# Kernel tuning notes

Measured on AMD Instinct MI355X. Metric: run time of the kernel, lower is better.

## Reference

```python
import jax, jax.numpy as jnp
import numpy as np

EPS = 1e-5
D_STATE = 16
D_INNER = 2
D_CONV = 4


def batchnorm(x, g, b):
    # BatchNorm1d in training mode: biased batch statistics over the batch dim
    m = x.mean(axis=0)
    v = x.var(axis=0)
    return g * (x - m) * jax.lax.rsqrt(v + EPS) + b


def mamba(u, W_in, conv_w, conv_b, W_xproj, W_dt, b_dt, A_log, D, W_out):
    # u: [B, L, 1] (d_model=1, d_inner=2, d_state=16, dt_rank=1)
    Bsz, L, _ = u.shape
    xz = jnp.einsum('bld,ed->ble', u, W_in)            # [B,L,4]
    x, z = jnp.split(xz, 2, axis=-1)                    # [B,L,2] each
    # causal depthwise conv along L
    xc = jnp.transpose(x, (0, 2, 1))                    # [B,C,L]
    xc = jax.lax.conv_general_dilated(
        xc, conv_w, (1,), [(D_CONV - 1, 0)],
        dimension_numbers=('NCH', 'OIH', 'NCH'),
        feature_group_count=D_INNER)
    x = jax.nn.silu(jnp.transpose(xc, (0, 2, 1)) + conv_b)  # [B,L,2]
    x_dbl = jnp.einsum('ble,fe->blf', x, W_xproj)       # [B,L,1+2*16]
    dt = jax.nn.softplus(jnp.einsum('blr,er->ble', x_dbl[..., :1], W_dt) + b_dt)  # [B,L,2]
    Bm = x_dbl[..., 1:1 + D_STATE]                      # [B,L,16]
    Cm = x_dbl[..., 1 + D_STATE:1 + 2 * D_STATE]        # [B,L,16]
    A = -jnp.exp(A_log)                                 # [2,16]

    def step(h, inp):
        dt_t, B_t, C_t, x_t = inp                       # [B,2],[B,16],[B,16],[B,2]
        dA = jnp.exp(dt_t[:, :, None] * A)              # [B,2,16]
        h = h * dA + dt_t[:, :, None] * B_t[:, None, :] * x_t[:, :, None]
        y = jnp.einsum('ben,bn->be', h, C_t) + D * x_t
        return h, y

    h0 = jnp.zeros((Bsz, D_INNER, D_STATE), u.dtype)
    xs = (dt.transpose(1, 0, 2), Bm.transpose(1, 0, 2),
          Cm.transpose(1, 0, 2), x.transpose(1, 0, 2))
    _, ys = jax.lax.scan(step, h0, xs)                  # [L,B,2]
    y = ys.transpose(1, 0, 2) * jax.nn.silu(z)          # [B,L,2]
    return jnp.einsum('ble,de->bld', y, W_out)          # [B,L,1]


def setup_inputs() -> dict:
    key = jax.random.key(0)
    ks = jax.random.split(key, 16)
    B = 1024
    s = 0.02
    inp = {
        'x': jax.random.normal(ks[0], (B, 1775), jnp.float32),
        'W1': jax.random.normal(ks[1], (2048, 1775), jnp.float32) * s,
        'g1': jnp.ones((2048,), jnp.float32),
        'b1': jnp.zeros((2048,), jnp.float32),
        'W_in': jax.random.normal(ks[2], (2 * D_INNER, 1), jnp.float32) * s,
        'conv_w': jax.random.normal(ks[3], (D_INNER, 1, D_CONV), jnp.float32) * 0.2,
        'conv_b': jnp.zeros((D_INNER,), jnp.float32),
        'W_xproj': jax.random.normal(ks[4], (1 + 2 * D_STATE, D_INNER), jnp.float32) * 0.2,
        'W_dt': jax.random.normal(ks[5], (D_INNER, 1), jnp.float32) * 0.2,
        'b_dt': jax.random.normal(ks[6], (D_INNER,), jnp.float32) * 0.2,
        'A_log': jnp.tile(jnp.log(jnp.arange(1, D_STATE + 1, dtype=jnp.float32)), (D_INNER, 1)),
        'D': jnp.ones((D_INNER,), jnp.float32),
        'W_out': jax.random.normal(ks[7], (1, D_INNER), jnp.float32) * 0.2,
        'W2': jax.random.normal(ks[8], (512, 2048), jnp.float32) * s,
        'g2': jnp.ones((512,), jnp.float32),
        'b2': jnp.zeros((512,), jnp.float32),
        'W3': jax.random.normal(ks[9], (256, 512), jnp.float32) * s,
    }
    return inp


def reference(x, W1, g1, b1, W_in, conv_w, conv_b, W_xproj, W_dt, b_dt,
              A_log, D, W_out, W2, g2, b2, W3):
    h = batchnorm(x @ W1.T, g1, b1)                     # [B,2048]
    h = mamba(h[:, :, None], W_in, conv_w, conv_b, W_xproj, W_dt, b_dt,
              A_log, D, W_out)[:, :, 0]                 # [B,2048]
    h = jax.nn.relu(batchnorm(h @ W2.T, g2, b2))        # [B,512]
    return h @ W3.T                                     # [B,256]
```

## Files before the change

kernel.cpp:

```cpp
#include <hip/hip_runtime.h>
#include <math.h>

#define SEQL 2048
#define BATCH 1024
#define CHUNK 64
#define NCH 32

typedef _Float16 f16x8 __attribute__((ext_vector_type(8)));
typedef _Float16 f16x4 __attribute__((ext_vector_type(4)));
typedef _Float16 h2 __attribute__((ext_vector_type(2)));
typedef float f32x4 __attribute__((ext_vector_type(4)));

__device__ inline unsigned short f2h(float f) {
    _Float16 h = (_Float16)f;
    return *reinterpret_cast<unsigned short*>(&h);
}
__device__ inline float packh2(float a, float b) {
    return __uint_as_float((unsigned)f2h(a) | ((unsigned)f2h(b) << 16));
}
__device__ inline float hext(float packed, int sh) {
    const unsigned short s = (unsigned short)(__float_as_uint(packed) >> sh);
    _Float16 h = *reinterpret_cast<const _Float16*>(&s);
    return (float)h;
}

__device__ inline void gl2lds16(const void* g, void* l) {
    __builtin_amdgcn_global_load_lds(
        (const __attribute__((address_space(1))) unsigned int*)g,
        (__attribute__((address_space(3))) unsigned int*)l, 16, 0, 0);
}

template<int CTRL>
__device__ inline float dppadd(float v) {
    const int p = __builtin_amdgcn_update_dpp(0, __float_as_int(v), CTRL, 0xF, 0xF, true);
    return v + __int_as_float(p);
}

__global__ __launch_bounds__(256) void cvt_all(
    const float* __restrict__ x, const float* __restrict__ W1,
    const float* __restrict__ W2, const float* __restrict__ W3,
    _Float16* __restrict__ xh, _Float16* __restrict__ w1h,
    _Float16* __restrict__ w2h, _Float16* __restrict__ w3h)
{
    const int bid = blockIdx.x;
    if (bid < 3072) {
        const float* src; _Float16* dst;
        if (bid < 1024) { src = x + (size_t)bid * 1775;           dst = xh  + (size_t)bid * 1792; }
        else            { src = W1 + (size_t)(bid - 1024) * 1775; dst = w1h + (size_t)(bid - 1024) * 1792; }
        f16x4* dst4 = reinterpret_cast<f16x4*>(dst);
        for (int i = threadIdx.x; i < 448; i += 256) {
            const int k = i * 4;
            float4 v = {0.f, 0.f, 0.f, 0.f};
            if (k + 3 < 1775) v = *reinterpret_cast<const float4*>(&src[k]);
            else {
                if (k     < 1775) v.x = src[k];
                if (k + 1 < 1775) v.y = src[k + 1];
                if (k + 2 < 1775) v.z = src[k + 2];
            }
            f16x4 o; o[0] = (_Float16)v.x; o[1] = (_Float16)v.y; o[2] = (_Float16)v.z; o[3] = (_Float16)v.w;
            dst4[i] = o;
        }
    } else {
        const float* src; _Float16* dst; int nvec;
        if (bid < 3584) { const int r = bid - 3072; src = W2 + (size_t)r * 2048; dst = w2h + (size_t)r * 2048; nvec = 512; }
        else            { const int r = bid - 3584; src = W3 + (size_t)r * 512;  dst = w3h + (size_t)r * 512;  nvec = 128; }
        f16x4* dst4 = reinterpret_cast<f16x4*>(dst);
        for (int i = threadIdx.x; i < nvec; i += 256) {
            const float4 v = reinterpret_cast<const float4*>(src)[i];
            f16x4 o; o[0] = (_Float16)v.x; o[1] = (_Float16)v.y; o[2] = (_Float16)v.z; o[3] = (_Float16)v.w;
            dst4[i] = o;
        }
    }
}

__global__ __launch_bounds__(256) void cvt_bnrelu(
    const float* __restrict__ P0, const float* __restrict__ P1,
    const float* __restrict__ sc, const float* __restrict__ tc,
    _Float16* __restrict__ h3)
{
    const int row = blockIdx.x * 2 + (threadIdx.x >> 7);
    const int i = threadIdx.x & 127;
    const float4 p0 = reinterpret_cast<const float4*>(P0 + (size_t)row * 512)[i];
    const float4 p1 = reinterpret_cast<const float4*>(P1 + (size_t)row * 512)[i];
    const float4 sv = reinterpret_cast<const float4*>(sc)[i];
    const float4 tv = reinterpret_cast<const float4*>(tc)[i];
    f16x4 o;
    o[0] = (_Float16)fmaxf(fmaf(sv.x, p0.x + p1.x, tv.x), 0.f);
    o[1] = (_Float16)fmaxf(fmaf(sv.y, p0.y + p1.y, tv.y), 0.f);
    o[2] = (_Float16)fmaxf(fmaf(sv.z, p0.z + p1.z, tv.z), 0.f);
    o[3] = (_Float16)fmaxf(fmaf(sv.w, p0.w + p1.w, tv.w), 0.f);
    reinterpret_cast<f16x4*>(h3 + (size_t)row * 512)[i] = o;
}

__global__ __launch_bounds__(256) void gemm_f16(
    const _Float16* __restrict__ A, const _Float16* __restrict__ B,
    float* __restrict__ C, int ldc, int Kp, int ksteps, size_t coff,
    float* __restrict__ bnp, int bn_ld)
{
    __shared__ __attribute__((aligned(16))) _Float16 sA[2][64 * 64];
    __shared__ __attribute__((aligned(16))) _Float16 sB[2][64 * 64];

    const int tid = threadIdx.x;
    const int wave = tid >> 6;
    const int lane = tid & 63;
    const int m0 = blockIdx.y * 64;
    const int n0 = blockIdx.x * 64;
    C += (size_t)blockIdx.z * coff;

    const int srow = tid >> 3;
    const int pslot = tid & 7;
    const int gslot = pslot ^ (srow & 7);
    const size_t gk0 = (size_t)blockIdx.z * ksteps * 64 + (size_t)gslot * 8;
    const _Float16* gA0 = A + (size_t)(m0 + srow) * Kp + gk0;
    const _Float16* gA1 = A + (size_t)(m0 + 32 + srow) * Kp + gk0;
    const _Float16* gB0 = B + (size_t)(n0 + srow) * Kp + gk0;
    const _Float16* gB1 = B + (size_t)(n0 + 32 + srow) * Kp + gk0;
    const int wdst = wave * 512;

    const int wr = wave >> 1, wc = wave & 1;
    const int li = lane & 15, gq = lane >> 4;
    const int p0s = (gq    ) ^ (li & 7);
    const int p1s = (gq + 4) ^ (li & 7);

    f32x4 acc[2][2];
    #pragma unroll
    for (int i = 0; i < 2; ++i)
        #pragma unroll
        for (int j = 0; j < 2; ++j)
            #pragma unroll
            for (int v = 0; v < 4; ++v) acc[i][j][v] = 0.f;

    gl2lds16(gA0, &sA[0][wdst]);
    gl2lds16(gA1, &sA[0][2048 + wdst]);
    gl2lds16(gB0, &sB[0][wdst]);
    gl2lds16(gB1, &sB[0][2048 + wdst]);
    __syncthreads();

    int cur = 0;
    for (int kt = 0; kt < ksteps; ++kt) {
        if (kt + 1 < ksteps) {
            const size_t go = (size_t)(kt + 1) * 64;
            const int nb = cur ^ 1;
            gl2lds16(gA0 + go, &sA[nb][wdst]);
            gl2lds16(gA1 + go, &sA[nb][2048 + wdst]);
            gl2lds16(gB0 + go, &sB[nb][wdst]);
            gl2lds16(gB1 + go, &sB[nb][2048 + wdst]);
        }

        f16x8 af[2][2], bg[2][2];
        #pragma unroll
        for (int mi = 0; mi < 2; ++mi) {
            const int rb = (wr * 32 + mi * 16 + li) * 64;
            af[mi][0] = *(const f16x8*)&sA[cur][rb + p0s * 8];
            af[mi][1] = *(const f16x8*)&sA[cur][rb + p1s * 8];
        }
        #pragma unroll
        for (int ni = 0; ni < 2; ++ni) {
            const int rb = (wc * 32 + ni * 16 + li) * 64;
            bg[ni][0] = *(const f16x8*)&sB[cur][rb + p0s * 8];
            bg[ni][1] = *(const f16x8*)&sB[cur][rb + p1s * 8];
        }
        #pragma unroll
        for (int mi = 0; mi < 2; ++mi)
            #pragma unroll
            for (int ni = 0; ni < 2; ++ni) {
                acc[mi][ni] = __builtin_amdgcn_mfma_f32_16x16x32_f16(af[mi][0], bg[ni][0], acc[mi][ni], 0, 0, 0);
                acc[mi][ni] = __builtin_amdgcn_mfma_f32_16x16x32_f16(af[mi][1], bg[ni][1], acc[mi][ni], 0, 0, 0);
            }
        __syncthreads();
        cur ^= 1;
    }

    #pragma unroll
    for (int mi = 0; mi < 2; ++mi)
        #pragma unroll
        for (int ni = 0; ni < 2; ++ni) {
            const int col = n0 + wc * 32 + ni * 16 + li;
            #pragma unroll
            for (int i = 0; i < 4; ++i) {
                const int row = m0 + wr * 32 + mi * 16 + gq * 4 + i;
                C[(size_t)row * ldc + col] = acc[mi][ni][i];
            }
        }

    if (bnp) {
        #pragma unroll
        for (int ni = 0; ni < 2; ++ni) {
            float ps = 0.f, pq = 0.f;
            #pragma unroll
            for (int mi = 0; mi < 2; ++mi)
                #pragma unroll
                for (int i = 0; i < 4; ++i) {
                    const float v = acc[mi][ni][i];
                    ps += v; pq += v * v;
                }
            ps += __shfl_xor(ps, 16); ps += __shfl_xor(ps, 32);
            pq += __shfl_xor(pq, 16); pq += __shfl_xor(pq, 32);
            if (gq == 0) {
                const int col = n0 + wc * 32 + ni * 16 + li;
                const int grp = blockIdx.y * 2 + wr;
                bnp[(size_t)(grp * 2    ) * bn_ld + col] = ps;
                bnp[(size_t)(grp * 2 + 1) * bn_ld + col] = pq;
            }
        }
    }
}

__global__ __launch_bounds__(256) void bn_part(
    const float* __restrict__ X, const float* __restrict__ X2,
    int rows_per, int ld, float* __restrict__ part)
{
    __shared__ float rs[4][64], rq[4][64];
    const int tid = threadIdx.x;
    const int c = tid & 63, rg4 = tid >> 6;
    const int col = blockIdx.x * 64 + c;
    const int r0 = blockIdx.y * rows_per;
    float sum = 0.f, sq = 0.f;
    for (int r = rg4; r < rows_per; r += 4) {
        const size_t idx = (size_t)(r0 + r) * ld + col;
        float v = X[idx];
        if (X2) v += X2[idx];
        sum += v; sq += v * v;
    }
    rs[rg4][c] = sum; rq[rg4][c] = sq;
    __syncthreads();
    if (rg4 == 0) {
        sum = rs[0][c] + rs[1][c] + rs[2][c] + rs[3][c];
        sq  = rq[0][c] + rq[1][c] + rq[2][c] + rq[3][c];
        part[((size_t)blockIdx.y * 2    ) * ld + col] = sum;
        part[((size_t)blockIdx.y * 2 + 1) * ld + col] = sq;
    }
}

__global__ __launch_bounds__(256) void bn_fin(
    const float* __restrict__ part, int RG, int ld, float inv_rows,
    const float* __restrict__ g, const float* __restrict__ b,
    float* __restrict__ s, float* __restrict__ t)
{
    const int col = blockIdx.x * 256 + threadIdx.x;
    if (col >= ld) return;
    float sum = 0.f, sq = 0.f;
    for (int z = 0; z < RG; ++z) {
        sum += part[((size_t)z * 2    ) * ld + col];
        sq  += part[((size_t)z * 2 + 1) * ld + col];
    }
    const float mean = sum * inv_rows;
    const float var = fmaxf(sq * inv_rows - mean * mean, 0.f);
    const float rstd = 1.0f / sqrtf(var + 1e-5f);
    const float sv = g[col] * rstd;
    s[col] = sv;
    t[col] = b[col] - mean * sv;
}

__global__ __launch_bounds__(512, 8) void mamba_scan9(
    const float* __restrict__ Y, _Float16* __restrict__ a2,
    const float* __restrict__ s1, const float* __restrict__ t1,
    const float* __restrict__ Win, const float* __restrict__ convw,
    const float* __restrict__ convb, const float* __restrict__ Wx,
    const float* __restrict__ Wdt, const float* __restrict__ bdt,
    const float* __restrict__ Alog, const float* __restrict__ Dp,
    const float* __restrict__ Wout)
{
    __shared__ __align__(16) float4 pk[SEQL];
    __shared__ float Pa[2][NCH][16];
    __shared__ float Sa[2][NCH][16];

    const int tid = threadIdx.x;
    const int row = blockIdx.x;
    const float* yrow = Y + (size_t)row * SEQL;
    _Float16* a2row = a2 + (size_t)row * SEQL;

    {
        const int l0 = tid * 4;
        float4 ym = {0.f,0.f,0.f,0.f}, sm = {0.f,0.f,0.f,0.f}, tm = {0.f,0.f,0.f,0.f};
        if (tid > 0) {
            ym = *reinterpret_cast<const float4*>(&yrow[l0 - 4]);
            sm = *reinterpret_cast<const float4*>(&s1[l0 - 4]);
            tm = *reinterpret_cast<const float4*>(&t1[l0 - 4]);
        }
        const float4 y0 = *reinterpret_cast<const float4*>(&yrow[l0]);
        const float4 s0 = *reinterpret_cast<const float4*>(&s1[l0]);
        const float4 t0 = *reinterpret_cast<const float4*>(&t1[l0]);

        float ua[8];
        ua[0] = fmaf(sm.x, ym.x, tm.x);
        ua[1] = fmaf(sm.y, ym.y, tm.y);
        ua[2] = fmaf(sm.z, ym.z, tm.z);
        ua[3] = fmaf(sm.w, ym.w, tm.w);
        ua[4] = fmaf(s0.x, y0.x, t0.x);
        ua[5] = fmaf(s0.y, y0.y, t0.y);
        ua[6] = fmaf(s0.z, y0.z, t0.z);
        ua[7] = fmaf(s0.w, y0.w, t0.w);

        const float wi0 = Win[0], wi1 = Win[1];
        const float wz0 = Win[2], wz1 = Win[3];
        const float wo0 = Wout[0], wo1 = Wout[1];
        const float cw00 = convw[0], cw01 = convw[1], cw02 = convw[2], cw03 = convw[3];
        const float cw10 = convw[4], cw11 = convw[5], cw12 = convw[6], cw13 = convw[7];
        const float cb0 = convb[0], cb1 = convb[1];
        const float wx00 = Wx[0], wx01 = Wx[1];
        const float wdt0 = Wdt[0], wdt1 = Wdt[1];
        const float bdt0 = bdt[0], bdt1 = bdt[1];

        #pragma unroll
        for (int j = 0; j < 4; ++j) {
            const int l = l0 + j;
            const float u0 = ua[j + 4], um1 = ua[j + 3], um2 = ua[j + 2], um3 = ua[j + 1];
            const float c0 = fmaf(wi0, cw00 * um3 + cw01 * um2 + cw02 * um1 + cw03 * u0, cb0);
            const float c1 = fmaf(wi1, cw10 * um3 + cw11 * um2 + cw12 * um1 + cw13 * u0, cb1);
            const float xs0 = c0 / (1.f + __expf(-c0));
            const float xs1 = c1 / (1.f + __expf(-c1));
            const float d0 = xs0 * wx00 + xs1 * wx01;
            const float dt0 = __logf(1.f + __expf(fmaf(d0, wdt0, bdt0)));
            const float dt1 = __logf(1.f + __expf(fmaf(d0, wdt1, bdt1)));
            const float z0 = u0 * wz0, z1 = u0 * wz1;
            const float g0 = (z0 / (1.f + __expf(-z0))) * wo0;
            const float g1 = (z1 / (1.f + __expf(-z1))) * wo1;
            float4 rec;
            rec.x = dt0; rec.y = dt1;
            rec.z = packh2(xs0, xs1);
            rec.w = packh2(g0, g1);
            pk[((l & 63) << 5) + (l >> 6)] = rec;
        }
    }
    __syncthreads();

    const int ch = tid >> 4;
    const int n  = tid & 15;

    const float A0 = -__expf(Alog[n])      * 1.44269504f;
    const float A1 = -__expf(Alog[16 + n]) * 1.44269504f;
    h2 wxB2, wxC2;
    wxB2[0] = (_Float16)Wx[(1 + n) * 2 + 0];
    wxB2[1] = (_Float16)Wx[(1 + n) * 2 + 1];
    wxC2[0] = (_Float16)Wx[(17 + n) * 2 + 0];
    wxC2[1] = (_Float16)Wx[(17 + n) * 2 + 1];

    {
        float h0 = 0.f, h1 = 0.f, p0 = 1.f, p1 = 1.f;
        for (int i0 = 0; i0 < CHUNK; i0 += 8) {
            #pragma unroll
            for (int j = 0; j < 8; ++j) {
                const float4 v = pk[((i0 + j) << 5) + ch];
                const h2 xs2 = __builtin_bit_cast(h2, v.z);
                const float Bn = __builtin_amdgcn_fdot2(xs2, wxB2, 0.f, false);
                const float xs0 = hext(v.z, 0), xs1 = hext(v.z, 16);
                const float dA0 = __builtin_amdgcn_exp2f(v.x * A0);
                const float dA1 = __builtin_amdgcn_exp2f(v.y * A1);
                h0 = fmaf(h0, dA0, (v.x * xs0) * Bn);
                h1 = fmaf(h1, dA1, (v.y * xs1) * Bn);
                p0 *= dA0; p1 *= dA1;
            }
        }
        Pa[0][ch][n] = p0; Pa[1][ch][n] = p1;
        Sa[0][ch][n] = h0; Sa[1][ch][n] = h1;
    }
    __syncthreads();

    if (tid < 32) {
        const int e = tid >> 4, nn = tid & 15;
        float H = 0.f;
        #pragma unroll
        for (int cc = 0; cc < NCH; ++cc) {
            const float Pv = Pa[e][cc][nn];
            const float Sv = Sa[e][cc][nn];
            Sa[e][cc][nn] = H;
            H = fmaf(Pv, H, Sv);
        }
    }
    __syncthreads();

    {
        h2 D2h;
        D2h[0] = (_Float16)Dp[0];
        D2h[1] = (_Float16)Dp[1];
        const int base = ch * CHUNK;
        float h0 = Sa[0][ch][n], h1 = Sa[1][ch][n];
        for (int i0 = 0; i0 < CHUNK; i0 += 8) {
            float qs[8];
            #pragma unroll
            for (int j = 0; j < 8; ++j) {
                const float4 v = pk[((i0 + j) << 5) + ch];
                const h2 xs2 = __builtin_bit_cast(h2, v.z);
                const h2 gg2 = __builtin_bit_cast(h2, v.w);
                const float Bn = __builtin_amdgcn_fdot2(xs2, wxB2, 0.f, false);
                const float Cn = __builtin_amdgcn_fdot2(xs2, wxC2, 0.f, false);
                const float xs0 = hext(v.z, 0), xs1 = hext(v.z, 16);
                const float g0 = hext(v.w, 0),  g1 = hext(v.w, 16);
                const float dA0 = __builtin_amdgcn_exp2f(v.x * A0);
                const float dA1 = __builtin_amdgcn_exp2f(v.y * A1);
                h0 = fmaf(h0, dA0, (v.x * xs0) * Bn);
                h1 = fmaf(h1, dA1, (v.y * xs1) * Bn);
                float t = h0 * g0;
                t = fmaf(h1, g1, t);
                float q = t * Cn;
                q = dppadd<0xB1>(q);
                q = dppadd<0x4E>(q);
                q = dppadd<0x141>(q);
                q = dppadd<0x140>(q);
                const h2 dgh = D2h * gg2;
                const float dterm = __builtin_amdgcn_fdot2(xs2, dgh, 0.f, false);
                qs[j] = q + dterm;
            }
            if (n == 0) {
                float4 st;
                st.x = __builtin_bit_cast(float, __builtin_amdgcn_cvt_pkrtz(qs[0], qs[1]));
                st.y = __builtin_bit_cast(float, __builtin_amdgcn_cvt_pkrtz(qs[2], qs[3]));
                st.z = __builtin_bit_cast(float, __builtin_amdgcn_cvt_pkrtz(qs[4], qs[5]));
                st.w = __builtin_bit_cast(float, __builtin_amdgcn_cvt_pkrtz(qs[6], qs[7]));
                *reinterpret_cast<float4*>(&a2row[base + i0]) = st;
            }
        }
    }
}

extern "C" void kernel_launch(void* const* d_in, const int* in_sizes, int n_in,
                              void* d_out, int out_size, void* d_ws, size_t ws_size,
                              hipStream_t stream)
{
    const float* x     = (const float*)d_in[0];
    const float* W1    = (const float*)d_in[1];
    const float* g1    = (const float*)d_in[2];
    const float* b1    = (const float*)d_in[3];
    const float* Win   = (const float*)d_in[4];
    const float* convw = (const float*)d_in[5];
    const float* convb = (const float*)d_in[6];
    const float* Wx    = (const float*)d_in[7];
    const float* Wdt   = (const float*)d_in[8];
    const float* bdt   = (const float*)d_in[9];
    const float* Alog  = (const float*)d_in[10];
    const float* Dp    = (const float*)d_in[11];
    const float* Wout  = (const float*)d_in[12];
    const float* W2    = (const float*)d_in[13];
    const float* g2    = (const float*)d_in[14];
    const float* b2    = (const float*)d_in[15];
    const float* W3    = (const float*)d_in[16];

    unsigned char* base = (unsigned char*)d_ws;
    float* C1 = (float*)(base + 0);
    float* P0 = (float*)(base + 8388608);
    float* P1 = (float*)(base + 10485760);
    float* s1 = (float*)(base + 12582912);
    float* t1 = (float*)(base + 12591104);
    float* s2 = (float*)(base + 12599296);
    float* t2 = (float*)(base + 12601344);
    float* bnp = (float*)(base + 12615680);
    _Float16* a2  = (_Float16*)(base + 13172736);
    _Float16* xh  = (_Float16*)(base + 17367040);
    _Float16* w1h = (_Float16*)(base + 21037056);
    _Float16* w2h = (_Float16*)(base + 28377088);
    _Float16* w3h = (_Float16*)(base + 30474240);
    _Float16* h3h = (_Float16*)(base + 30736384);

    cvt_all<<<3840, 256, 0, stream>>>(x, W1, W2, W3, xh, w1h, w2h, w3h);

    gemm_f16<<<dim3(32, 16, 1), 256, 0, stream>>>(
        xh, w1h, C1, 2048, 1792, 28, 0, bnp, 2048);

    bn_fin<<<8, 256, 0, stream>>>(bnp, 32, 2048, 1.0f / 1024.f, g1, b1, s1, t1);

    mamba_scan9<<<1024, 512, 0, stream>>>(C1, a2, s1, t1, Win, convw, convb,
                                          Wx, Wdt, bdt, Alog, Dp, Wout);

    gemm_f16<<<dim3(8, 16, 2), 256, 0, stream>>>(
        a2, w2h, P0, 512, 2048, 16, (size_t)1024 * 512, nullptr, 0);

    bn_part<<<dim3(8, 16), 256, 0, stream>>>(P0, P1, 64, 512, bnp);
    bn_fin<<<2, 256, 0, stream>>>(bnp, 16, 512, 1.0f / 1024.f, g2, b2, s2, t2);

    cvt_bnrelu<<<512, 256, 0, stream>>>(P0, P1, s2, t2, h3h);

    gemm_f16<<<dim3(4, 16, 1), 256, 0, stream>>>(
        h3h, w3h, (float*)d_out, 256, 512, 8, 0, nullptr, 0);
}
```

Measured before the change: 126.8 us.

## Fuse BN2 finalize, split-K reduce, ReLU and fp16 cast into final GEMM

Replaces the bn_fin, cvt_bnrelu and last gemm_f16 launches with one kernel. Each block recomputes the BN2 scale and shift from the partial sums into LDS, then reads the two split-K fp32 partials, applies scale, shift and ReLU, and casts to fp16 while staging the A tile. This saves two launches and the fp16 intermediate round trip through memory. In exchange, every block repeats the statistics reduction and reads fp32 A data at twice the bytes, with the conversion on the load path.

```diff
diff --git a/kernel.cpp b/kernel.cpp
--- a/kernel.cpp
+++ b/kernel.cpp
@@ -73,25 +73,6 @@
     }
 }
 
-__global__ __launch_bounds__(256) void cvt_bnrelu(
-    const float* __restrict__ P0, const float* __restrict__ P1,
-    const float* __restrict__ sc, const float* __restrict__ tc,
-    _Float16* __restrict__ h3)
-{
-    const int row = blockIdx.x * 2 + (threadIdx.x >> 7);
-    const int i = threadIdx.x & 127;
-    const float4 p0 = reinterpret_cast<const float4*>(P0 + (size_t)row * 512)[i];
-    const float4 p1 = reinterpret_cast<const float4*>(P1 + (size_t)row * 512)[i];
-    const float4 sv = reinterpret_cast<const float4*>(sc)[i];
-    const float4 tv = reinterpret_cast<const float4*>(tc)[i];
-    f16x4 o;
-    o[0] = (_Float16)fmaxf(fmaf(sv.x, p0.x + p1.x, tv.x), 0.f);
-    o[1] = (_Float16)fmaxf(fmaf(sv.y, p0.y + p1.y, tv.y), 0.f);
-    o[2] = (_Float16)fmaxf(fmaf(sv.z, p0.z + p1.z, tv.z), 0.f);
-    o[3] = (_Float16)fmaxf(fmaf(sv.w, p0.w + p1.w, tv.w), 0.f);
-    reinterpret_cast<f16x4*>(h3 + (size_t)row * 512)[i] = o;
-}
-
 __global__ __launch_bounds__(256) void gemm_f16(
     const _Float16* __restrict__ A, const _Float16* __restrict__ B,
     float* __restrict__ C, int ldc, int Kp, int ksteps, size_t coff,
@@ -204,6 +185,152 @@
             }
         }
     }
+}
+
+__global__ __launch_bounds__(256) void gemm3_fused(
+    const float* __restrict__ P0, const float* __restrict__ P1,
+    const float* __restrict__ bnp,
+    const float* __restrict__ g2, const float* __restrict__ b2,
+    const _Float16* __restrict__ B, float* __restrict__ C)
+{
+    __shared__ __attribute__((aligned(16))) _Float16 sA[2][64 * 64];
+    __shared__ __attribute__((aligned(16))) _Float16 sB[2][64 * 64];
+    __shared__ __attribute__((aligned(16))) float s2l[512];
+    __shared__ __attribute__((aligned(16))) float t2l[512];
+
+    const int tid = threadIdx.x;
+    const int wave = tid >> 6;
+    const int lane = tid & 63;
+    const int m0 = blockIdx.y * 64;
+    const int n0 = blockIdx.x * 64;
+
+    const int srow = tid >> 3;
+    const int pslot = tid & 7;
+    const int gslot = pslot ^ (srow & 7);
+    const int wslot = gslot * 8;
+    const _Float16* gB0 = B + (size_t)(n0 + srow) * 512 + gslot * 8;
+    const _Float16* gB1 = B + (size_t)(n0 + 32 + srow) * 512 + gslot * 8;
+    const int wdst = wave * 512;
+
+    const float* gP00 = P0 + (size_t)(m0 + srow) * 512 + pslot * 8;
+    const float* gP01 = P0 + (size_t)(m0 + 32 + srow) * 512 + pslot * 8;
+    const float* gP10 = P1 + (size_t)(m0 + srow) * 512 + pslot * 8;
+    const float* gP11 = P1 + (size_t)(m0 + 32 + srow) * 512 + pslot * 8;
+
+    for (int c = tid; c < 512; c += 256) {
+        float sum = 0.f, sq = 0.f;
+        #pragma unroll
+        for (int z = 0; z < 16; ++z) {
+            sum += bnp[(size_t)(z * 2    ) * 512 + c];
+            sq  += bnp[(size_t)(z * 2 + 1) * 512 + c];
+        }
+        const float mean = sum * (1.0f / 1024.f);
+        const float var = fmaxf(sq * (1.0f / 1024.f) - mean * mean, 0.f);
+        const float rstd = 1.0f / sqrtf(var + 1e-5f);
+        const float sv = g2[c] * rstd;
+        s2l[c] = sv;
+        t2l[c] = b2[c] - mean * sv;
+    }
+
+    auto stageA = [&](int kt, int b) {
+        const int kc = kt * 64 + pslot * 8;
+        const float4 a0 = *reinterpret_cast<const float4*>(gP00 + kt * 64);
+        const float4 a1 = *reinterpret_cast<const float4*>(gP00 + kt * 64 + 4);
+        const float4 c0 = *reinterpret_cast<const float4*>(gP10 + kt * 64);
+        const float4 c1 = *reinterpret_cast<const float4*>(gP10 + kt * 64 + 4);
+        const float4 d0 = *reinterpret_cast<const float4*>(gP01 + kt * 64);
+        const float4 d1 = *reinterpret_cast<const float4*>(gP01 + kt * 64 + 4);
+        const float4 e0 = *reinterpret_cast<const float4*>(gP11 + kt * 64);
+        const float4 e1 = *reinterpret_cast<const float4*>(gP11 + kt * 64 + 4);
+        const float4 sv0 = *reinterpret_cast<const float4*>(&s2l[kc]);
+        const float4 sv1 = *reinterpret_cast<const float4*>(&s2l[kc + 4]);
+        const float4 tv0 = *reinterpret_cast<const float4*>(&t2l[kc]);
+        const float4 tv1 = *reinterpret_cast<const float4*>(&t2l[kc + 4]);
+        f16x8 o;
+        o[0] = (_Float16)fmaxf(fmaf(sv0.x, a0.x + c0.x, tv0.x), 0.f);
+        o[1] = (_Float16)fmaxf(fmaf(sv0.y, a0.y + c0.y, tv0.y), 0.f);
+        o[2] = (_Float16)fmaxf(fmaf(sv0.z, a0.z + c0.z, tv0.z), 0.f);
+        o[3] = (_Float16)fmaxf(fmaf(sv0.w, a0.w + c0.w, tv0.w), 0.f);
+        o[4] = (_Float16)fmaxf(fmaf(sv1.x, a1.x + c1.x, tv1.x), 0.f);
+        o[5] = (_Float16)fmaxf(fmaf(sv1.y, a1.y + c1.y, tv1.y), 0.f);
+        o[6] = (_Float16)fmaxf(fmaf(sv1.z, a1.z + c1.z, tv1.z), 0.f);
+        o[7] = (_Float16)fmaxf(fmaf(sv1.w, a1.w + c1.w, tv1.w), 0.f);
+        *reinterpret_cast<f16x8*>(&sA[b][srow * 64 + wslot]) = o;
+        f16x8 p;
+        p[0] = (_Float16)fmaxf(fmaf(sv0.x, d0.x + e0.x, tv0.x), 0.f);
+        p[1] = (_Float16)fmaxf(fmaf(sv0.y, d0.y + e0.y, tv0.y), 0.f);
+        p[2] = (_Float16)fmaxf(fmaf(sv0.z, d0.z + e0.z, tv0.z), 0.f);
+        p[3] = (_Float16)fmaxf(fmaf(sv0.w, d0.w + e0.w, tv0.w), 0.f);
+        p[4] = (_Float16)fmaxf(fmaf(sv1.x, d1.x + e1.x, tv1.x), 0.f);
+        p[5] = (_Float16)fmaxf(fmaf(sv1.y, d1.y + e1.y, tv1.y), 0.f);
+        p[6] = (_Float16)fmaxf(fmaf(sv1.z, d1.z + e1.z, tv1.z), 0.f);
+        p[7] = (_Float16)fmaxf(fmaf(sv1.w, d1.w + e1.w, tv1.w), 0.f);
+        *reinterpret_cast<f16x8*>(&sA[b][(srow + 32) * 64 + wslot]) = p;
+    };
+
+    const int wr = wave >> 1, wc = wave & 1;
+    const int li = lane & 15, gq = lane >> 4;
+    const int p0s = (gq    ) ^ (li & 7);
+    const int p1s = (gq + 4) ^ (li & 7);
+
+    f32x4 acc[2][2];
+    #pragma unroll
+    for (int i = 0; i < 2; ++i)
+        #pragma unroll
+        for (int j = 0; j < 2; ++j)
+            #pragma unroll
+            for (int v = 0; v < 4; ++v) acc[i][j][v] = 0.f;
+
+    gl2lds16(gB0, &sB[0][wdst]);
+    gl2lds16(gB1, &sB[0][2048 + wdst]);
+    __syncthreads();
+    stageA(0, 0);
+    __syncthreads();
+
+    int cur = 0;
+    for (int kt = 0; kt < 8; ++kt) {
+        if (kt + 1 < 8) {
+            const int nb = cur ^ 1;
+            gl2lds16(gB0 + (size_t)(kt + 1) * 64, &sB[nb][wdst]);
+            gl2lds16(gB1 + (size_t)(kt + 1) * 64, &sB[nb][2048 + wdst]);
+            stageA(kt + 1, nb);
+        }
+
+        f16x8 af[2][2], bg[2][2];
+        #pragma unroll
+        for (int mi = 0; mi < 2; ++mi) {
+            const int rb = (wr * 32 + mi * 16 + li) * 64;
+            af[mi][0] = *(const f16x8*)&sA[cur][rb + p0s * 8];
+            af[mi][1] = *(const f16x8*)&sA[cur][rb + p1s * 8];
+        }
+        #pragma unroll
+        for (int ni = 0; ni < 2; ++ni) {
+            const int rb = (wc * 32 + ni * 16 + li) * 64;
+            bg[ni][0] = *(const f16x8*)&sB[cur][rb + p0s * 8];
+            bg[ni][1] = *(const f16x8*)&sB[cur][rb + p1s * 8];
+        }
+        #pragma unroll
+        for (int mi = 0; mi < 2; ++mi)
+            #pragma unroll
+            for (int ni = 0; ni < 2; ++ni) {
+                acc[mi][ni] = __builtin_amdgcn_mfma_f32_16x16x32_f16(af[mi][0], bg[ni][0], acc[mi][ni], 0, 0, 0);
+                acc[mi][ni] = __builtin_amdgcn_mfma_f32_16x16x32_f16(af[mi][1], bg[ni][1], acc[mi][ni], 0, 0, 0);
+            }
+        __syncthreads();
+        cur ^= 1;
+    }
+
+    #pragma unroll
+    for (int mi = 0; mi < 2; ++mi)
+        #pragma unroll
+        for (int ni = 0; ni < 2; ++ni) {
+            const int col = n0 + wc * 32 + ni * 16 + li;
+            #pragma unroll
+            for (int i = 0; i < 4; ++i) {
+                const int row = m0 + wr * 32 + mi * 16 + gq * 4 + i;
+                C[(size_t)row * 256 + col] = acc[mi][ni][i];
+            }
+        }
 }
 
 __global__ __launch_bounds__(256) void bn_part(
@@ -442,15 +569,12 @@
     float* P1 = (float*)(base + 10485760);
     float* s1 = (float*)(base + 12582912);
     float* t1 = (float*)(base + 12591104);
-    float* s2 = (float*)(base + 12599296);
-    float* t2 = (float*)(base + 12601344);
     float* bnp = (float*)(base + 12615680);
     _Float16* a2  = (_Float16*)(base + 13172736);
     _Float16* xh  = (_Float16*)(base + 17367040);
     _Float16* w1h = (_Float16*)(base + 21037056);
     _Float16* w2h = (_Float16*)(base + 28377088);
     _Float16* w3h = (_Float16*)(base + 30474240);
-    _Float16* h3h = (_Float16*)(base + 30736384);
 
     cvt_all<<<3840, 256, 0, stream>>>(x, W1, W2, W3, xh, w1h, w2h, w3h);
 
@@ -466,10 +590,7 @@
         a2, w2h, P0, 512, 2048, 16, (size_t)1024 * 512, nullptr, 0);
 
     bn_part<<<dim3(8, 16), 256, 0, stream>>>(P0, P1, 64, 512, bnp);
-    bn_fin<<<2, 256, 0, stream>>>(bnp, 16, 512, 1.0f / 1024.f, g2, b2, s2, t2);
-
-    cvt_bnrelu<<<512, 256, 0, stream>>>(P0, P1, s2, t2, h3h);
-
-    gemm_f16<<<dim3(4, 16, 1), 256, 0, stream>>>(
-        h3h, w3h, (float*)d_out, 256, 512, 8, 0, nullptr, 0);
-}
+
+    gemm3_fused<<<dim3(4, 16), 256, 0, stream>>>(
+        P0, P1, bnp, g2, b2, w3h, (float*)d_out);
+}
```

After: 123.9 us. 2.3% less time.
